# Optimization experiments

Hardware: AMD Instinct MI355X
Metric: run time of the kernel (lower is better)

Reference implementation:

```python
import jax, jax.numpy as jnp
import numpy as np

NUM_CLASSES = 80
BATCH_PER_IMG = 512
FG_CAP = 128  # int(512 * 0.25)
IOU_THRESH = 0.5
STRIDE = 16.0
OUT = 7
RATIO = 2


def _pairwise_iou(gt, pr):
    # gt: [M,4], pr: [N,4] in (x1,y1,x2,y2) -> [M,N]
    area_g = (gt[:, 2] - gt[:, 0]) * (gt[:, 3] - gt[:, 1])
    area_p = (pr[:, 2] - pr[:, 0]) * (pr[:, 3] - pr[:, 1])
    lt = jnp.maximum(gt[:, None, :2], pr[None, :, :2])
    rb = jnp.minimum(gt[:, None, 2:], pr[None, :, 2:])
    wh = jnp.clip(rb - lt, 0.0)
    inter = wh[..., 0] * wh[..., 1]
    union = area_g[:, None] + area_p[None, :] - inter
    return jnp.where(inter > 0, inter / union, 0.0)


def _match_and_sample(iou, gt_cls, rand):
    # iou: [M,N]; Matcher(thresholds=[0.5], labels=[0,1], no low-quality)
    matched_vals = iou.max(axis=0)
    matched_idxs = iou.argmax(axis=0)
    matched = matched_vals >= IOU_THRESH
    cls = jnp.where(matched, gt_cls[matched_idxs], NUM_CLASSES)
    fg = cls != NUM_CLASSES
    bg = ~fg

    def _rank(mask):
        # rank of each masked element under random permutation (rand in [0,1))
        key = jnp.where(mask, rand, 2.0)
        return jnp.argsort(jnp.argsort(key))

    num_fg = jnp.minimum(fg.sum(), FG_CAP)
    sel_fg = fg & (_rank(fg) < num_fg)
    num_bg = jnp.minimum(BATCH_PER_IMG - num_fg, bg.sum())
    sel_bg = bg & (_rank(bg) < num_bg)
    score = sel_fg * 2.0 + sel_bg * 1.0
    _, sampled = jax.lax.top_k(score, BATCH_PER_IMG)
    return sampled, cls[sampled], matched_idxs[sampled]


def _roi_align(feat, rois, batch_idx):
    # feat: [B,C,H,W], rois: [R,4] image coords, aligned=True ROIAlignV2
    B, C, H, W = feat.shape
    f = feat.transpose(0, 2, 3, 1)  # [B,H,W,C]
    b = rois / STRIDE - 0.5
    x1, y1, x2, y2 = b[:, 0], b[:, 1], b[:, 2], b[:, 3]
    g = (jnp.arange(OUT * RATIO, dtype=feat.dtype) + 0.5) / RATIO  # [14] in bin units
    xs = x1[:, None] + g[None, :] * ((x2 - x1) / OUT)[:, None]  # [R,14]
    ys = y1[:, None] + g[None, :] * ((y2 - y1) / OUT)[:, None]
    xs = jnp.clip(xs, 0.0, W - 1)
    ys = jnp.clip(ys, 0.0, H - 1)
    x0 = jnp.floor(xs).astype(jnp.int32)
    y0 = jnp.floor(ys).astype(jnp.int32)
    x1i = jnp.minimum(x0 + 1, W - 1)
    y1i = jnp.minimum(y0 + 1, H - 1)
    lx = xs - x0.astype(xs.dtype)
    ly = ys - y0.astype(ys.dtype)
    bb = batch_idx[:, None, None]
    v00 = f[bb, y0[:, :, None], x0[:, None, :]]  # [R,14,14,C]
    v01 = f[bb, y0[:, :, None], x1i[:, None, :]]
    v10 = f[bb, y1i[:, :, None], x0[:, None, :]]
    v11 = f[bb, y1i[:, :, None], x1i[:, None, :]]
    wy1 = ly[:, :, None, None]
    wy0 = 1.0 - wy1
    wx1 = lx[:, None, :, None]
    wx0 = 1.0 - wx1
    val = v00 * wy0 * wx0 + v01 * wy0 * wx1 + v10 * wy1 * wx0 + v11 * wy1 * wx1
    R = rois.shape[0]
    pooled = val.reshape(R, OUT, RATIO, OUT, RATIO, C).mean(axis=(2, 4))  # [R,7,7,C]
    return pooled.transpose(0, 3, 1, 2).reshape(R, -1)  # channel-major flatten, matches torch


def setup_inputs() -> dict:
    key = jax.random.key(0)
    ks = jax.random.split(key, 14)
    B, N, M, C, H, W = 2, 2000, 64, 256, 64, 64
    IMG = 1024.0

    def mk_boxes(k, b, n):
        pts = jax.random.uniform(k, (b, n, 2, 2), jnp.float32) * (IMG - 16.0)
        lo = pts.min(axis=2)
        hi = pts.max(axis=2) + 8.0
        return jnp.concatenate([lo, hi], axis=-1)

    D = C * OUT * OUT  # 12544
    FC = 1024
    return {
        "features": jax.random.normal(ks[0], (B, C, H, W), jnp.float32),
        "proposal_boxes": mk_boxes(ks[1], B, N),
        "gt_boxes": mk_boxes(ks[2], B, M),
        "gt_classes": jax.random.randint(ks[3], (B, M), 0, NUM_CLASSES),
        "rand_scores": jax.random.uniform(ks[4], (B, N + M), jnp.float32),
        "fc1_w": jax.random.normal(ks[5], (D, FC), jnp.float32) * 0.02,
        "fc1_b": jnp.zeros((FC,), jnp.float32),
        "fc2_w": jax.random.normal(ks[6], (FC, FC), jnp.float32) * 0.02,
        "fc2_b": jnp.zeros((FC,), jnp.float32),
        "cls_w": jax.random.normal(ks[7], (FC, NUM_CLASSES + 1), jnp.float32) * 0.02,
        "cls_b": jnp.zeros((NUM_CLASSES + 1,), jnp.float32),
        "box_w": jax.random.normal(ks[8], (FC, NUM_CLASSES * 4), jnp.float32) * 0.02,
        "box_b": jnp.zeros((NUM_CLASSES * 4,), jnp.float32),
    }


def reference(features, proposal_boxes, gt_boxes, gt_classes, rand_scores,
              fc1_w, fc1_b, fc2_w, fc2_b, cls_w, cls_b, box_w, box_b):
    # proposal_append_gt: concat GT boxes onto proposals
    all_boxes = jnp.concatenate([proposal_boxes, gt_boxes], axis=1)  # [B,N+M,4]
    iou = jax.vmap(_pairwise_iou)(gt_boxes, all_boxes)  # [B,M,N+M]
    sampled, cls, _ = jax.vmap(_match_and_sample)(iou, gt_classes, rand_scores)
    rois = jnp.take_along_axis(all_boxes, sampled[..., None], axis=1).reshape(-1, 4)
    B = features.shape[0]
    bidx = jnp.repeat(jnp.arange(B), BATCH_PER_IMG)
    x = _roi_align(features, rois, bidx)  # [R, 12544]
    x = jax.nn.relu(x @ fc1_w + fc1_b)
    x = jax.nn.relu(x @ fc2_w + fc2_b)
    out = jnp.concatenate([x @ cls_w + cls_b, x @ box_w + box_b], axis=-1)  # [R, 401]
    return out
```

## Files before the change

### kernel.cpp

```cpp
#include <hip/hip_runtime.h>
#include <cstdint>
#include <cstddef>

constexpr int B_   = 2;
constexpr int N_   = 2000;
constexpr int M_   = 64;
constexpr int NB_  = N_ + M_;
constexpr int C_   = 256;
constexpr int H_   = 64;
constexpr int W_   = 64;
constexpr int RPI  = 512;
constexpr int RTOT = B_ * RPI;
constexpr int FG_CAP_ = 128;
constexpr int D_   = C_ * 49;
constexpr int FC_  = 1024;
constexpr int OUTC = 401;
constexpr int KT1  = D_ / 32;
constexpr int KT2  = FC_ / 32;
constexpr float IOU_T = 0.5f;

typedef _Float16 f16;
typedef f16   f16x8 __attribute__((ext_vector_type(8)));
typedef float f32x4 __attribute__((ext_vector_type(4)));

__device__ __forceinline__ void tile_load16(const void* g, void* l) {
  __builtin_amdgcn_global_load_lds(
      (const __attribute__((address_space(1))) unsigned int*)g,
      (__attribute__((address_space(3))) unsigned int*)l, 16, 0, 0);
}

__global__ __launch_bounds__(256) void k_transpose(const float* __restrict__ in,
                                                   float* __restrict__ out) {
  __shared__ float tile[32][33];
  int b = blockIdx.z, hw0 = blockIdx.x * 32, c0 = blockIdx.y * 32;
  int tx = threadIdx.x, ty = threadIdx.y;
#pragma unroll
  for (int i = ty; i < 32; i += 8)
    tile[i][tx] = in[((size_t)b * C_ + c0 + i) * (H_ * W_) + hw0 + tx];
  __syncthreads();
#pragma unroll
  for (int i = ty; i < 32; i += 8)
    out[((size_t)b * (H_ * W_) + hw0 + i) * C_ + c0 + tx] = tile[tx][i];
}

__global__ __launch_bounds__(1024) void k_iou(const float* __restrict__ prop,
                                              const float* __restrict__ gt,
                                              unsigned char* __restrict__ fg,
                                              int* __restrict__ cnt) {
  __shared__ float s_gt[M_ * 4];
  __shared__ float s_area[M_];
  __shared__ int s_cnt;
  int b = blockIdx.x, t = threadIdx.x;
  if (t == 0) s_cnt = 0;
  if (t < M_ * 4) s_gt[t] = gt[(size_t)b * M_ * 4 + t];
  __syncthreads();
  if (t < M_) {
    float x1 = s_gt[t*4], y1 = s_gt[t*4+1], x2 = s_gt[t*4+2], y2 = s_gt[t*4+3];
    s_area[t] = (x2 - x1) * (y2 - y1);
  }
  __syncthreads();
  int local = 0;
  for (int j = t; j < NB_; j += 1024) {
    float bx1, by1, bx2, by2;
    if (j < N_) {
      const float* p = prop + ((size_t)b * N_ + j) * 4;
      bx1 = p[0]; by1 = p[1]; bx2 = p[2]; by2 = p[3];
    } else {
      const float* p = s_gt + (j - N_) * 4;
      bx1 = p[0]; by1 = p[1]; bx2 = p[2]; by2 = p[3];
    }
    float area_p = (bx2 - bx1) * (by2 - by1);
    float best = 0.f;
    for (int g = 0; g < M_; ++g) {
      float lx = fmaxf(s_gt[g*4], bx1),   lyv = fmaxf(s_gt[g*4+1], by1);
      float rx = fminf(s_gt[g*4+2], bx2), ry  = fminf(s_gt[g*4+3], by2);
      float w = fmaxf(rx - lx, 0.f), h = fmaxf(ry - lyv, 0.f);
      float inter = w * h;
      float iou = inter > 0.f ? inter / (s_area[g] + area_p - inter) : 0.f;
      best = fmaxf(best, iou);
    }
    int f = (best >= IOU_T) ? 1 : 0;
    fg[(size_t)b * NB_ + j] = (unsigned char)f;
    local += f;
  }
  atomicAdd(&s_cnt, local);
  __syncthreads();
  if (t == 0) cnt[b] = s_cnt;
}

__global__ __launch_bounds__(256) void k_rank(const float* __restrict__ rnd,
                                              const unsigned char* __restrict__ fg,
                                              const int* __restrict__ cnt,
                                              unsigned char* __restrict__ sel) {
  __shared__ unsigned long long s_key[NB_];
  int b = blockIdx.y, t = threadIdx.x;
  for (int j = t; j < NB_; j += 256) {
    float r = rnd[(size_t)b * NB_ + j];
    int f = (int)fg[(size_t)b * NB_ + j];
    float ck = r + 2.0f * (float)f;
    unsigned int ib = __float_as_uint(ck);
    s_key[j] = ((unsigned long long)ib << 11) | (unsigned int)j;
  }
  __syncthreads();
  int j = blockIdx.x * 256 + t;
  int jj = (j < NB_) ? j : 0;
  unsigned long long uj = s_key[jj];
  int rank_all = 0;
  const uint4* kp = (const uint4*)s_key;
#pragma unroll 4
  for (int k2 = 0; k2 < NB_ / 2; ++k2) {
    uint4 v = kp[k2];
    unsigned long long k0 = ((unsigned long long)v.y << 32) | v.x;
    unsigned long long k1 = ((unsigned long long)v.w << 32) | v.z;
    rank_all += (k0 < uj) ? 1 : 0;
    rank_all += (k1 < uj) ? 1 : 0;
  }
  if (j >= NB_) return;
  int fgcnt  = cnt[b];
  int num_fg = min(fgcnt, FG_CAP_);
  int num_bg = min(RPI - num_fg, NB_ - fgcnt);
  int myfg   = (uj >> 11) >= 0x40000000ull ? 1 : 0;
  int rank   = rank_all - (myfg ? (NB_ - fgcnt) : 0);
  int lim    = myfg ? num_fg : num_bg;
  sel[(size_t)b * NB_ + j] =
      (rank < lim) ? (unsigned char)(myfg ? 2 : 1) : (unsigned char)0;
}

__global__ __launch_bounds__(64) void k_place(const float* __restrict__ prop,
                                              const float* __restrict__ gt,
                                              const int* __restrict__ cnt,
                                              const unsigned char* __restrict__ sel,
                                              float* __restrict__ rois) {
  int b = blockIdx.x, L = threadIdx.x;
  int fgcnt  = cnt[b];
  int num_fg = min(fgcnt, FG_CAP_);
  int num_bg = min(RPI - num_fg, NB_ - fgcnt);
  int S = num_fg + num_bg;
  int t2 = 0, t1 = 0, t0 = 0;
  unsigned long long lt = (L == 0) ? 0ull : ((~0ull) >> (64 - L));
  for (int c = 0; c < (NB_ + 63) / 64; ++c) {
    int j = c * 64 + L;
    int s = (j < NB_) ? (int)sel[(size_t)b * NB_ + j] : -1;
    unsigned long long m2 = __ballot(s == 2);
    unsigned long long m1 = __ballot(s == 1);
    unsigned long long m0 = __ballot(s == 0);
    int pos = -1;
    if (s == 2) {
      pos = t2 + __popcll(m2 & lt);
    } else if (s == 1) {
      pos = num_fg + t1 + __popcll(m1 & lt);
    } else if (s == 0) {
      int p0 = t0 + __popcll(m0 & lt);
      if (S + p0 < RPI) pos = S + p0;
    }
    if (pos >= 0) {
      const float* p = (j < N_) ? (prop + ((size_t)b * N_ + j) * 4)
                                : (gt + ((size_t)b * M_ + (j - N_)) * 4);
      float* o = rois + ((size_t)b * RPI + pos) * 4;
      o[0] = p[0]; o[1] = p[1]; o[2] = p[2]; o[3] = p[3];
    }
    t2 += __popcll(m2); t1 += __popcll(m1); t0 += __popcll(m0);
  }
}

__global__ __launch_bounds__(256) void k_roialign(const float* __restrict__ fT,
                                                  const float* __restrict__ rois,
                                                  f16* __restrict__ Ahi,
                                                  f16* __restrict__ Alo) {
  __shared__ float sv[8][257];
  int bin = blockIdx.x, mt = blockIdx.y;
  int c = threadIdx.x;
  int by = bin / 7, bx = bin % 7;
  for (int pass = 0; pass < 2; ++pass) {
    for (int r8 = 0; r8 < 8; ++r8) {
      int r = mt * 16 + pass * 8 + r8;
      const float* rp = rois + (size_t)r * 4;
      float x1 = rp[0] * 0.0625f - 0.5f;
      float y1 = rp[1] * 0.0625f - 0.5f;
      float x2 = rp[2] * 0.0625f - 0.5f;
      float y2 = rp[3] * 0.0625f - 0.5f;
      float stx = (x2 - x1) * (1.0f / 7.0f);
      float sty = (y2 - y1) * (1.0f / 7.0f);
      const float* fb = fT + (size_t)(r >> 9) * H_ * W_ * C_;
      float acc = 0.f;
#pragma unroll
      for (int s = 0; s < 4; ++s) {
        int oy = s >> 1, ox = s & 1;
        float xs = x1 + ((float)(2 * bx + ox) + 0.5f) * 0.5f * stx;
        float ys = y1 + ((float)(2 * by + oy) + 0.5f) * 0.5f * sty;
        xs = fminf(fmaxf(xs, 0.f), (float)(W_ - 1));
        ys = fminf(fmaxf(ys, 0.f), (float)(H_ - 1));
        int x0 = (int)floorf(xs), y0 = (int)floorf(ys);
        int x1i = min(x0 + 1, W_ - 1), y1i = min(y0 + 1, H_ - 1);
        float lx = xs - (float)x0, ly = ys - (float)y0;
        float v00 = fb[((size_t)y0 * W_ + x0) * C_ + c];
        float v01 = fb[((size_t)y0 * W_ + x1i) * C_ + c];
        float v10 = fb[((size_t)y1i * W_ + x0) * C_ + c];
        float v11 = fb[((size_t)y1i * W_ + x1i) * C_ + c];
        acc += v00*(1.f-ly)*(1.f-lx) + v01*(1.f-ly)*lx + v10*ly*(1.f-lx) + v11*ly*lx;
      }
      sv[r8][c] = acc * 0.25f;
    }
    __syncthreads();
    int kt   = c >> 5;
    int l5   = c & 31;
    int quad = l5 >> 3;
    int r8   = l5 & 7;
    int lane = quad * 16 + pass * 8 + r8;
    int cbase = kt * 32 + quad * 8;
    f16x8 hv, lv;
#pragma unroll
    for (int jj = 0; jj < 8; ++jj) {
      float v = sv[r8][cbase + jj];
      f16 h = (f16)v;
      hv[jj] = h;
      lv[jj] = (f16)(v - (float)h);
    }
    size_t off = ((size_t)(mt * KT1 + bin * 8 + kt) * 64 + lane) * 8;
    *(f16x8*)(Ahi + off) = hv;
    *(f16x8*)(Alo + off) = lv;
    __syncthreads();
  }
}

__global__ __launch_bounds__(256) void k_convw(const float* __restrict__ src,
                                               const float* __restrict__ src2,
                                               f16* __restrict__ dst,
                                               int KTtot, int mode) {
  int q = blockIdx.x * 256 + threadIdx.x;
  int lane = q & 63, tile = q >> 6;
  int nt = tile / KTtot, kt = tile - nt * KTtot;
  int n  = nt * 16 + (lane & 15);
  int k0 = kt * 32 + (lane >> 4) * 8;
  f16x8 h;
#pragma unroll
  for (int jj = 0; jj < 8; ++jj) {
    int k = k0 + jj;
    float v;
    if (mode == 0) {
      v = src[(size_t)k * 1024 + n];
    } else if (mode == 1) {
      int row = (k & 255) * 49 + (k >> 8);
      v = src[(size_t)row * 1024 + n];
    } else {
      v = (n < 81) ? src[(size_t)k * 81 + n]
                   : ((n < 401) ? src2[(size_t)k * 320 + (n - 81)] : 0.f);
    }
    h[jj] = (f16)v;
  }
  *(f16x8*)(dst + (size_t)q * 8) = h;
}

__global__ __launch_bounds__(256, 2) void k_gemm_mfma(
    const f16* __restrict__ Ahi, const f16* __restrict__ Alo,
    const f16* __restrict__ Bw, float* __restrict__ P,
    int N, int KTtot, int ktPerSplit) {
  __shared__ f16 sAh[8 * 512];
  __shared__ f16 sAl[8 * 512];
  __shared__ f16 sB[8 * 512];
  int tid = threadIdx.x;
  int lane = tid & 63, w = tid >> 6;
  int wm = w >> 1, wn = w & 1;
  int bm = blockIdx.x, bn = blockIdx.y, z = blockIdx.z;
  int kt0 = z * ktPerSplit, ktEnd = kt0 + ktPerSplit;

  f32x4 acc[4][4];
#pragma unroll
  for (int i = 0; i < 4; ++i)
#pragma unroll
    for (int j = 0; j < 4; ++j) {
      f32x4 zv = {0.f, 0.f, 0.f, 0.f};
      acc[i][j] = zv;
    }

  for (int kt = kt0; kt < ktEnd; ++kt) {
#pragma unroll
    for (int tt = 0; tt < 6; ++tt) {
      int t = 6 * w + tt;
      const f16* g;
      f16* l;
      if (t < 8)       { g = Ahi + ((size_t)(bm*8 + t)      * KTtot + kt) * 512; l = sAh + t * 512; }
      else if (t < 16) { g = Alo + ((size_t)(bm*8 + (t-8))  * KTtot + kt) * 512; l = sAl + (t-8) * 512; }
      else             { g = Bw  + ((size_t)(bn*8 + (t-16)) * KTtot + kt) * 512; l = sB  + (t-16) * 512; }
      tile_load16(g + lane * 8, l);
    }
    __syncthreads();
    f16x8 ah[4], al[4], bw[4];
#pragma unroll
    for (int i = 0; i < 4; ++i) {
      ah[i] = *(const f16x8*)(sAh + (wm*4 + i) * 512 + lane * 8);
      al[i] = *(const f16x8*)(sAl + (wm*4 + i) * 512 + lane * 8);
      bw[i] = *(const f16x8*)(sB  + (wn*4 + i) * 512 + lane * 8);
    }
#pragma unroll
    for (int i = 0; i < 4; ++i)
#pragma unroll
      for (int j = 0; j < 4; ++j) {
        acc[i][j] = __builtin_amdgcn_mfma_f32_16x16x32_f16(ah[i], bw[j], acc[i][j], 0, 0, 0);
        acc[i][j] = __builtin_amdgcn_mfma_f32_16x16x32_f16(al[i], bw[j], acc[i][j], 0, 0, 0);
      }
    __syncthreads();
  }

  int quad = lane >> 4, cl = lane & 15;
  float* Pz = P + (size_t)z * 1024 * (size_t)N;
#pragma unroll
  for (int i = 0; i < 4; ++i) {
    int row = bm * 128 + wm * 64 + i * 16 + quad * 4;
#pragma unroll
    for (int j = 0; j < 4; ++j) {
      int col = bn * 128 + wn * 64 + j * 16 + cl;
#pragma unroll
      for (int r = 0; r < 4; ++r)
        Pz[(size_t)(row + r) * N + col] = acc[i][j][r];
    }
  }
}

__global__ __launch_bounds__(256) void k_combine(const float* __restrict__ P,
                                                 const float* __restrict__ bias,
                                                 f16* __restrict__ Ahi,
                                                 f16* __restrict__ Alo,
                                                 int nsplit) {
  int q = blockIdx.x * 256 + threadIdx.x;
  int lane = q & 63, tile = q >> 6;
  int mt = tile >> 5, kt = tile & 31;
  int m  = mt * 16 + (lane & 15);
  int n0 = kt * 32 + (lane >> 4) * 8;
  float v[8];
#pragma unroll
  for (int jj = 0; jj < 8; ++jj) v[jj] = bias[n0 + jj];
  for (int s = 0; s < nsplit; ++s) {
    const float* p = P + (size_t)s * 1048576 + (size_t)m * 1024 + n0;
#pragma unroll
    for (int jj = 0; jj < 8; ++jj) v[jj] += p[jj];
  }
  f16x8 hv, lv;
#pragma unroll
  for (int jj = 0; jj < 8; ++jj) {
    float x = fmaxf(v[jj], 0.f);
    f16 h = (f16)x;
    hv[jj] = h;
    lv[jj] = (f16)(x - (float)h);
  }
  *(f16x8*)(Ahi + (size_t)q * 8) = hv;
  *(f16x8*)(Alo + (size_t)q * 8) = lv;
}

__global__ __launch_bounds__(256) void k_out(const float* __restrict__ P,
                                             const float* __restrict__ cls_b,
                                             const float* __restrict__ box_b,
                                             float* __restrict__ out, int nsplit) {
  int idx = blockIdx.x * 256 + threadIdx.x;
  if (idx >= RTOT * OUTC) return;
  int m = idx / OUTC, n = idx - m * OUTC;
  float v = (n < 81) ? cls_b[n] : box_b[n - 81];
  for (int s = 0; s < nsplit; ++s)
    v += P[(size_t)s * (1024 * 512) + (size_t)m * 512 + n];
  out[idx] = v;
}

extern "C" void kernel_launch(void* const* d_in, const int* in_sizes, int n_in,
                              void* d_out, int out_size, void* d_ws, size_t ws_size,
                              hipStream_t stream) {
  const float* features = (const float*)d_in[0];
  const float* prop     = (const float*)d_in[1];
  const float* gt       = (const float*)d_in[2];
  const float* rnd      = (const float*)d_in[4];
  const float* fc1_w    = (const float*)d_in[5];
  const float* fc1_b    = (const float*)d_in[6];
  const float* fc2_w    = (const float*)d_in[7];
  const float* fc2_b    = (const float*)d_in[8];
  const float* cls_w    = (const float*)d_in[9];
  const float* cls_b    = (const float*)d_in[10];
  const float* box_w    = (const float*)d_in[11];
  const float* box_b    = (const float*)d_in[12];
  float* out = (float*)d_out;

  char* base = (char*)d_ws;
  float* fT   = (float*)(base + 0);
  float* rois = (float*)(base + 8388608);
  char*  p2   = base + 8404992;
  f16* A1hi = (f16*)(base + 8404992);
  f16* A1lo = (f16*)(base + 34095104);
  f16* W1   = (f16*)(base + 59785216);
  float* P1 = (float*)(base + 85475328);
  int s1 = (ws_size >= (size_t)85475328 + 8ull * 4194304) ? 8 : 4;
  f16* A2hi = (f16*)(p2 + 0);
  f16* A2lo = (f16*)(p2 + 2097152);
  f16* W2   = (f16*)(p2 + 4194304);
  f16* A3hi = (f16*)(p2 + 6291456);
  f16* A3lo = (f16*)(p2 + 8388608);
  f16* W3   = (f16*)(p2 + 10485760);
  float* P2 = (float*)(p2 + 11534336);
  float* P3 = (float*)(p2 + 45088768);
  unsigned char* g_fg  = (unsigned char*)(base + 85475328);
  unsigned char* g_sel = (unsigned char*)(base + 85475328 + 4160);
  int*           g_cnt = (int*)(base + 85475328 + 8320);

  k_transpose<<<dim3(128, 8, B_), dim3(32, 8), 0, stream>>>(features, fT);
  k_iou<<<dim3(B_), dim3(1024), 0, stream>>>(prop, gt, g_fg, g_cnt);
  k_rank<<<dim3((NB_ + 255) / 256, B_), dim3(256), 0, stream>>>(rnd, g_fg, g_cnt, g_sel);
  k_place<<<dim3(B_), dim3(64), 0, stream>>>(prop, gt, g_cnt, g_sel, rois);
  k_roialign<<<dim3(49, 64), dim3(256), 0, stream>>>(fT, rois, A1hi, A1lo);
  k_convw<<<dim3(6272), dim3(256), 0, stream>>>(fc1_w, nullptr, W1, KT1, 1);
  k_gemm_mfma<<<dim3(8, 8, s1), dim3(256), 0, stream>>>(A1hi, A1lo, W1, P1,
                                                        1024, KT1, KT1 / s1);
  k_combine<<<dim3(512), dim3(256), 0, stream>>>(P1, fc1_b, A2hi, A2lo, s1);
  k_convw<<<dim3(512), dim3(256), 0, stream>>>(fc2_w, nullptr, W2, KT2, 0);
  k_gemm_mfma<<<dim3(8, 8, 8), dim3(256), 0, stream>>>(A2hi, A2lo, W2, P2,
                                                       1024, KT2, KT2 / 8);
  k_combine<<<dim3(512), dim3(256), 0, stream>>>(P2, fc2_b, A3hi, A3lo, 8);
  k_convw<<<dim3(256), dim3(256), 0, stream>>>(cls_w, box_w, W3, KT2, 2);
  k_gemm_mfma<<<dim3(8, 4, 4), dim3(256), 0, stream>>>(A3hi, A3lo, W3, P3,
                                                       512, KT2, KT2 / 4);
  k_out<<<dim3((RTOT * OUTC + 255) / 256), dim3(256), 0, stream>>>(
      P3, cls_b, box_b, out, 4);
}
```

Baseline: 359.4 us.

## Drop fp16 hi/lo activation split and coalesce weight conversion via LDS tile

Activations are now stored as a single fp16 copy instead of a hi+lo split pair. This halves the MFMA count, the A-tile LDS traffic and the activation writes across all three GEMMs. Weight conversion now stages a 32x64 tile in shared memory so global reads are coalesced along n rather than strided along k. The FC2 split-K factor also drops from 8 to 4. The price is accuracy: activations lose the lo correction term, which may put results closer to the tolerance limit.

```diff
diff --git a/kernel.cpp b/kernel.cpp
--- a/kernel.cpp
+++ b/kernel.cpp
@@ -165,8 +165,7 @@
 
 __global__ __launch_bounds__(256) void k_roialign(const float* __restrict__ fT,
                                                   const float* __restrict__ rois,
-                                                  f16* __restrict__ Ahi,
-                                                  f16* __restrict__ Alo) {
+                                                  f16* __restrict__ Ahi) {
   __shared__ float sv[8][257];
   int bin = blockIdx.x, mt = blockIdx.y;
   int c = threadIdx.x;
@@ -208,17 +207,11 @@
     int r8   = l5 & 7;
     int lane = quad * 16 + pass * 8 + r8;
     int cbase = kt * 32 + quad * 8;
-    f16x8 hv, lv;
-#pragma unroll
-    for (int jj = 0; jj < 8; ++jj) {
-      float v = sv[r8][cbase + jj];
-      f16 h = (f16)v;
-      hv[jj] = h;
-      lv[jj] = (f16)(v - (float)h);
-    }
+    f16x8 hv;
+#pragma unroll
+    for (int jj = 0; jj < 8; ++jj) hv[jj] = (f16)sv[r8][cbase + jj];
     size_t off = ((size_t)(mt * KT1 + bin * 8 + kt) * 64 + lane) * 8;
     *(f16x8*)(Ahi + off) = hv;
-    *(f16x8*)(Alo + off) = lv;
     __syncthreads();
   }
 }
@@ -227,36 +220,43 @@
                                                const float* __restrict__ src2,
                                                f16* __restrict__ dst,
                                                int KTtot, int mode) {
-  int q = blockIdx.x * 256 + threadIdx.x;
-  int lane = q & 63, tile = q >> 6;
-  int nt = tile / KTtot, kt = tile - nt * KTtot;
-  int n  = nt * 16 + (lane & 15);
-  int k0 = kt * 32 + (lane >> 4) * 8;
-  f16x8 h;
-#pragma unroll
-  for (int jj = 0; jj < 8; ++jj) {
-    int k = k0 + jj;
+  __shared__ float tile[32][65];
+  int kt = blockIdx.x, ng = blockIdx.y;
+  int t = threadIdx.x;
+  int n0 = ng * 64;
+  int col = t & 63;
+#pragma unroll
+  for (int p = 0; p < 8; ++p) {
+    int r = p * 4 + (t >> 6);
+    int k = kt * 32 + r;
     float v;
     if (mode == 0) {
-      v = src[(size_t)k * 1024 + n];
+      v = src[(size_t)k * 1024 + n0 + col];
     } else if (mode == 1) {
       int row = (k & 255) * 49 + (k >> 8);
-      v = src[(size_t)row * 1024 + n];
+      v = src[(size_t)row * 1024 + n0 + col];
     } else {
+      int n = n0 + col;
       v = (n < 81) ? src[(size_t)k * 81 + n]
                    : ((n < 401) ? src2[(size_t)k * 320 + (n - 81)] : 0.f);
     }
-    h[jj] = (f16)v;
-  }
-  *(f16x8*)(dst + (size_t)q * 8) = h;
+    tile[r][col] = v;
+  }
+  __syncthreads();
+  int sub = t >> 6, lane = t & 63;
+  int nt = ng * 4 + sub;
+  int nl = lane & 15, kg = lane >> 4;
+  f16x8 h;
+#pragma unroll
+  for (int e = 0; e < 8; ++e)
+    h[e] = (f16)tile[kg * 8 + e][sub * 16 + nl];
+  *(f16x8*)(dst + ((size_t)(nt * KTtot + kt) * 64 + lane) * 8) = h;
 }
 
 __global__ __launch_bounds__(256, 2) void k_gemm_mfma(
-    const f16* __restrict__ Ahi, const f16* __restrict__ Alo,
-    const f16* __restrict__ Bw, float* __restrict__ P,
-    int N, int KTtot, int ktPerSplit) {
+    const f16* __restrict__ Ahi, const f16* __restrict__ Bw,
+    float* __restrict__ P, int N, int KTtot, int ktPerSplit) {
   __shared__ f16 sAh[8 * 512];
-  __shared__ f16 sAl[8 * 512];
   __shared__ f16 sB[8 * 512];
   int tid = threadIdx.x;
   int lane = tid & 63, w = tid >> 6;
@@ -275,30 +275,26 @@
 
   for (int kt = kt0; kt < ktEnd; ++kt) {
 #pragma unroll
-    for (int tt = 0; tt < 6; ++tt) {
-      int t = 6 * w + tt;
+    for (int tt = 0; tt < 4; ++tt) {
+      int t = 4 * w + tt;
       const f16* g;
       f16* l;
-      if (t < 8)       { g = Ahi + ((size_t)(bm*8 + t)      * KTtot + kt) * 512; l = sAh + t * 512; }
-      else if (t < 16) { g = Alo + ((size_t)(bm*8 + (t-8))  * KTtot + kt) * 512; l = sAl + (t-8) * 512; }
-      else             { g = Bw  + ((size_t)(bn*8 + (t-16)) * KTtot + kt) * 512; l = sB  + (t-16) * 512; }
+      if (t < 8) { g = Ahi + ((size_t)(bm*8 + t)     * KTtot + kt) * 512; l = sAh + t * 512; }
+      else       { g = Bw  + ((size_t)(bn*8 + (t-8)) * KTtot + kt) * 512; l = sB + (t-8) * 512; }
       tile_load16(g + lane * 8, l);
     }
     __syncthreads();
-    f16x8 ah[4], al[4], bw[4];
+    f16x8 ah[4], bw[4];
 #pragma unroll
     for (int i = 0; i < 4; ++i) {
       ah[i] = *(const f16x8*)(sAh + (wm*4 + i) * 512 + lane * 8);
-      al[i] = *(const f16x8*)(sAl + (wm*4 + i) * 512 + lane * 8);
       bw[i] = *(const f16x8*)(sB  + (wn*4 + i) * 512 + lane * 8);
     }
 #pragma unroll
     for (int i = 0; i < 4; ++i)
 #pragma unroll
-      for (int j = 0; j < 4; ++j) {
+      for (int j = 0; j < 4; ++j)
         acc[i][j] = __builtin_amdgcn_mfma_f32_16x16x32_f16(ah[i], bw[j], acc[i][j], 0, 0, 0);
-        acc[i][j] = __builtin_amdgcn_mfma_f32_16x16x32_f16(al[i], bw[j], acc[i][j], 0, 0, 0);
-      }
     __syncthreads();
   }
 
@@ -320,7 +316,6 @@
 __global__ __launch_bounds__(256) void k_combine(const float* __restrict__ P,
                                                  const float* __restrict__ bias,
                                                  f16* __restrict__ Ahi,
-                                                 f16* __restrict__ Alo,
                                                  int nsplit) {
   int q = blockIdx.x * 256 + threadIdx.x;
   int lane = q & 63, tile = q >> 6;
@@ -335,16 +330,10 @@
 #pragma unroll
     for (int jj = 0; jj < 8; ++jj) v[jj] += p[jj];
   }
-  f16x8 hv, lv;
-#pragma unroll
-  for (int jj = 0; jj < 8; ++jj) {
-    float x = fmaxf(v[jj], 0.f);
-    f16 h = (f16)x;
-    hv[jj] = h;
-    lv[jj] = (f16)(x - (float)h);
-  }
+  f16x8 hv;
+#pragma unroll
+  for (int jj = 0; jj < 8; ++jj) hv[jj] = (f16)fmaxf(v[jj], 0.f);
   *(f16x8*)(Ahi + (size_t)q * 8) = hv;
-  *(f16x8*)(Alo + (size_t)q * 8) = lv;
 }
 
 __global__ __launch_bounds__(256) void k_out(const float* __restrict__ P,
@@ -382,37 +371,34 @@
   float* rois = (float*)(base + 8388608);
   char*  p2   = base + 8404992;
   f16* A1hi = (f16*)(base + 8404992);
-  f16* A1lo = (f16*)(base + 34095104);
-  f16* W1   = (f16*)(base + 59785216);
-  float* P1 = (float*)(base + 85475328);
-  int s1 = (ws_size >= (size_t)85475328 + 8ull * 4194304) ? 8 : 4;
+  f16* W1   = (f16*)(base + 34095104);
+  float* P1 = (float*)(base + 59785216);
+  int s1 = (ws_size >= (size_t)59785216 + 8ull * 4194304) ? 8 : 4;
   f16* A2hi = (f16*)(p2 + 0);
-  f16* A2lo = (f16*)(p2 + 2097152);
-  f16* W2   = (f16*)(p2 + 4194304);
-  f16* A3hi = (f16*)(p2 + 6291456);
-  f16* A3lo = (f16*)(p2 + 8388608);
-  f16* W3   = (f16*)(p2 + 10485760);
-  float* P2 = (float*)(p2 + 11534336);
-  float* P3 = (float*)(p2 + 45088768);
-  unsigned char* g_fg  = (unsigned char*)(base + 85475328);
-  unsigned char* g_sel = (unsigned char*)(base + 85475328 + 4160);
-  int*           g_cnt = (int*)(base + 85475328 + 8320);
+  f16* W2   = (f16*)(p2 + 2097152);
+  f16* A3hi = (f16*)(p2 + 4194304);
+  f16* W3   = (f16*)(p2 + 6291456);
+  float* P2 = (float*)(p2 + 7340032);
+  float* P3 = (float*)(p2 + 24117248);
+  unsigned char* g_fg  = (unsigned char*)(base + 59785216);
+  unsigned char* g_sel = (unsigned char*)(base + 59785216 + 4160);
+  int*           g_cnt = (int*)(base + 59785216 + 8320);
 
   k_transpose<<<dim3(128, 8, B_), dim3(32, 8), 0, stream>>>(features, fT);
   k_iou<<<dim3(B_), dim3(1024), 0, stream>>>(prop, gt, g_fg, g_cnt);
   k_rank<<<dim3((NB_ + 255) / 256, B_), dim3(256), 0, stream>>>(rnd, g_fg, g_cnt, g_sel);
   k_place<<<dim3(B_), dim3(64), 0, stream>>>(prop, gt, g_cnt, g_sel, rois);
-  k_roialign<<<dim3(49, 64), dim3(256), 0, stream>>>(fT, rois, A1hi, A1lo);
-  k_convw<<<dim3(6272), dim3(256), 0, stream>>>(fc1_w, nullptr, W1, KT1, 1);
-  k_gemm_mfma<<<dim3(8, 8, s1), dim3(256), 0, stream>>>(A1hi, A1lo, W1, P1,
+  k_roialign<<<dim3(49, 64), dim3(256), 0, stream>>>(fT, rois, A1hi);
+  k_convw<<<dim3(KT1, 16), dim3(256), 0, stream>>>(fc1_w, nullptr, W1, KT1, 1);
+  k_gemm_mfma<<<dim3(8, 8, s1), dim3(256), 0, stream>>>(A1hi, W1, P1,
                                                         1024, KT1, KT1 / s1);
-  k_combine<<<dim3(512), dim3(256), 0, stream>>>(P1, fc1_b, A2hi, A2lo, s1);
-  k_convw<<<dim3(512), dim3(256), 0, stream>>>(fc2_w, nullptr, W2, KT2, 0);
-  k_gemm_mfma<<<dim3(8, 8, 8), dim3(256), 0, stream>>>(A2hi, A2lo, W2, P2,
-                                                       1024, KT2, KT2 / 8);
-  k_combine<<<dim3(512), dim3(256), 0, stream>>>(P2, fc2_b, A3hi, A3lo, 8);
-  k_convw<<<dim3(256), dim3(256), 0, stream>>>(cls_w, box_w, W3, KT2, 2);
-  k_gemm_mfma<<<dim3(8, 4, 4), dim3(256), 0, stream>>>(A3hi, A3lo, W3, P3,
+  k_combine<<<dim3(512), dim3(256), 0, stream>>>(P1, fc1_b, A2hi, s1);
+  k_convw<<<dim3(KT2, 16), dim3(256), 0, stream>>>(fc2_w, nullptr, W2, KT2, 0);
+  k_gemm_mfma<<<dim3(8, 8, 4), dim3(256), 0, stream>>>(A2hi, W2, P2,
+                                                       1024, KT2, KT2 / 4);
+  k_combine<<<dim3(512), dim3(256), 0, stream>>>(P2, fc2_b, A3hi, 4);
+  k_convw<<<dim3(KT2, 8), dim3(256), 0, stream>>>(cls_w, box_w, W3, KT2, 2);
+  k_gemm_mfma<<<dim3(8, 4, 4), dim3(256), 0, stream>>>(A3hi, W3, P3,
                                                        512, KT2, KT2 / 4);
   k_out<<<dim3((RTOT * OUTC + 255) / 256), dim3(256), 0, stream>>>(
       P3, cls_b, box_b, out, 4);
```

After: 351.6 us. -2.2%, faster.
